# Performance work log

Hardware: AMD Instinct MI355X
Metric: run time of the kernel (lower is better)

## Reference

```python
import jax, jax.numpy as jnp
import numpy as np

N_FFT = 2048
HOP = 512
OUT_CH = N_FFT // 2 + 1  # 1025


def _dft_conv_weights():
    # periodic ('fftbins=True') Hann window, win_length == n_fft so no padding
    n = np.arange(N_FFT)
    window = 0.5 - 0.5 * np.cos(2.0 * np.pi * n / N_FFT)
    k = np.arange(OUT_CH)
    ang = 2.0 * np.pi * np.outer(k, n) / N_FFT  # (OUT_CH, N_FFT)
    w_real = (np.cos(ang) * window[None, :]).astype(np.float32)
    w_imag = (-np.sin(ang) * window[None, :]).astype(np.float32)
    return jnp.asarray(w_real), jnp.asarray(w_imag)


def setup_inputs() -> dict:
    key = jax.random.key(0)
    x = jax.random.normal(key, (32, 2, 160000), dtype=jnp.float32)
    W_real, W_imag = _dft_conv_weights()
    return {"x": x, "W_real": W_real, "W_imag": W_imag}


def reference(x, W_real, W_imag):
    # x: (B, C, L). center=True -> reflect pad by n_fft//2 on both sides.
    pad = N_FFT // 2
    x_pad = jnp.pad(x, ((0, 0), (0, 0), (pad, pad)), mode="reflect")
    L = x_pad.shape[-1]
    num_frames = (L - N_FFT) // HOP + 1  # 313
    # frame indices: (T, N_FFT)
    idx = jnp.arange(num_frames)[:, None] * HOP + jnp.arange(N_FFT)[None, :]
    frames = x_pad[..., idx]  # (B, C, T, N_FFT)
    # windowed DFT as matmul (equivalent to the Conv1d with stride=hop)
    real = jnp.einsum("bctn,kn->bctk", frames, W_real)
    imag = jnp.einsum("bctn,kn->bctk", frames, W_imag)
    return real, imag
```

## Files before the change

### kernel.cpp

```cpp
#include <hip/hip_runtime.h>

#define B_     32
#define C_     2
#define L_     160000
#define HOP    512
#define PAD    1024
#define LPAD   162048
#define T_     313
#define BC     64
#define M_     20032
#define KCH    1025
#define OUT_HALF 20532800UL
#define PL     81024
#define KD     1024
#define ND     1024
#define NKT    32
#define MTP    160
#define NWG    1280
#define LIMW   8336

typedef __attribute__((ext_vector_type(8))) short short8;
typedef __attribute__((ext_vector_type(4))) float f32x4;

static __device__ __forceinline__ short f2bf(float f) {
  union { float f; unsigned u; } v; v.f = f;
  unsigned u = v.u;
  unsigned r = (u + 0x7fffu + ((u >> 16) & 1u)) >> 16;
  return (short)r;
}

__global__ void prep_planes(const float* __restrict__ x,
                            short* __restrict__ pl0, short* __restrict__ pl1) {
  int v = blockIdx.x * 256 + threadIdx.x;
  int bc = v / 10128;
  int r  = v - bc * 10128;
  int p0 = r * 8;
  const float* src = x + (size_t)bc * L_;
  short8 e, o;
  if (r >= 64 && r <= 10000) {
    int j0 = 16 * r - 1024;
    #pragma unroll
    for (int qq = 0; qq < 4; ++qq) {
      float4 f = *(const float4*)(src + j0 + qq * 4);
      e[qq * 2 + 0] = f2bf(f.x); o[qq * 2 + 0] = f2bf(f.y);
      e[qq * 2 + 1] = f2bf(f.z); o[qq * 2 + 1] = f2bf(f.w);
    }
  } else {
    #pragma unroll
    for (int u = 0; u < 16; ++u) {
      int j = 16 * r + u - 1024;
      j = j < 0 ? -j : j;
      j = j >= L_ ? 2 * L_ - 2 - j : j;
      short b = f2bf(src[j]);
      if (u & 1) o[u >> 1] = b; else e[u >> 1] = b;
    }
  }
  *(short8*)&pl0[(size_t)bc * PL + p0] = e;
  *(short8*)&pl1[(size_t)bc * PL + p0] = o;
}

__global__ void prep_wb(short* __restrict__ wb0, short* __restrict__ wb1) {
  int id = blockIdx.x * 256 + threadIdx.x;
  int s   = id >> 17;
  int row = (id >> 7) & 1023;
  int n8  = (id & 127) * 8;
  int kp  = row >> 1, e = row & 1;
  short8 ov;
  #pragma unroll
  for (int u = 0; u < 8; ++u) {
    int n1 = n8 + u;
    float win = 0.5f - 0.5f * cosf((float)(2 * n1 + s) * 3.0679615757712823e-3f);
    float tw;
    if (e == 0)       tw = cosf((float)((n1 * kp) & 1023) * 6.1359231515425649e-3f);
    else if (kp == 0) tw = (n1 & 1) ? -1.0f : 1.0f;
    else              tw = -sinf((float)((n1 * kp) & 1023) * 6.1359231515425649e-3f);
    ov[u] = f2bf(win * tw);
  }
  short* wb = s ? wb1 : wb0;
  *(short8*)&wb[(size_t)row * KD + n8] = ov;
}

#define GLOAD16(g, l) __builtin_amdgcn_global_load_lds(                        \
    (const __attribute__((address_space(1))) void*)(g),                        \
    (__attribute__((address_space(3))) void*)(l), 16, 0, 0)

__global__ __launch_bounds__(512, 4) void stft_gemm(const short* __restrict__ pl0,
                                                    const short* __restrict__ pl1,
                                                    const short* __restrict__ wb0,
                                                    const short* __restrict__ wb1,
                                                    float* __restrict__ out) {
  __shared__ __align__(16) char lds[66688];
  const int tid  = threadIdx.x;
  const int lane = tid & 63;
  const int wid  = tid >> 6;

  const int id = blockIdx.x;
  const int mt = (id & 7) * 20 + (id >> 6);
  const int nt = (id >> 3) & 7;
  const int M0 = mt * 128, N0 = nt * 128;

  const int srow = tid >> 2;
  const int chunkSwz = ((tid & 3) ^ ((tid >> 3) & 3)) * 8;
  const short* aP[2];
  const short* bP[2];
  {
    int m = M0 + srow; if (m > M_ - 1) m = M_ - 1;
    int bc = m / T_;
    int t  = m - bc * T_;
    size_t base = (size_t)bc * PL + (size_t)t * 256 + chunkSwz;
    aP[0] = pl0 + base;
    aP[1] = pl1 + base;
    size_t bb = (size_t)(N0 + srow) * KD + chunkSwz;
    bP[0] = wb0 + bb;
    bP[1] = wb1 + bb;
  }
  const int dstOff = tid * 16;

  const int wr = wid >> 2, wc = wid & 3;
  const int fr = lane & 15;
  const int xorb = ((lane >> 4) * 16) ^ ((fr & 6) << 3);
  int afOff[2][4], bfOff[2][2];
  #pragma unroll
  for (int s = 0; s < 2; ++s) {
    #pragma unroll
    for (int i = 0; i < 4; ++i)
      afOff[s][i] = s * 8192 + (wr * 64 + i * 16 + fr) * 64 + xorb;
    #pragma unroll
    for (int j = 0; j < 2; ++j)
      bfOff[s][j] = 16384 + s * 8192 + (wc * 32 + j * 16 + fr) * 64 + xorb;
  }

  f32x4 acc[2][4][2];
  #pragma unroll
  for (int s = 0; s < 2; ++s)
    #pragma unroll
    for (int i = 0; i < 4; ++i)
      #pragma unroll
      for (int j = 0; j < 2; ++j) acc[s][i][j] = (f32x4){0.f, 0.f, 0.f, 0.f};

  GLOAD16(aP[0], lds + dstOff);
  GLOAD16(bP[0], lds + 16384 + dstOff);
  GLOAD16(aP[1], lds + 8192 + dstOff);
  GLOAD16(bP[1], lds + 24576 + dstOff);

  for (int kt = 0; kt < NKT; ++kt) {
    char* bufR = lds + (kt & 1) * 32768;
    char* bufW = lds + ((kt + 1) & 1) * 32768;
    const int kos = (kt + 1) * 32;
    const bool st = (kt < NKT - 1);

    asm volatile("s_waitcnt vmcnt(2)" ::: "memory");
    __builtin_amdgcn_s_barrier();
    if (st) {
      GLOAD16(aP[0] + kos, bufW + dstOff);
      GLOAD16(bP[0] + kos, bufW + 16384 + dstOff);
    }
    short8 af0[4], bf0[2];
    #pragma unroll
    for (int i = 0; i < 4; ++i) af0[i] = *(const short8*)(bufR + afOff[0][i]);
    #pragma unroll
    for (int j = 0; j < 2; ++j) bf0[j] = *(const short8*)(bufR + bfOff[0][j]);
    __builtin_amdgcn_s_barrier();
    __builtin_amdgcn_s_setprio(1);
    #pragma unroll
    for (int i = 0; i < 4; ++i)
      #pragma unroll
      for (int j = 0; j < 2; ++j)
        acc[0][i][j] = __builtin_amdgcn_mfma_f32_16x16x32_bf16(af0[i], bf0[j],
                                                               acc[0][i][j], 0, 0, 0);
    __builtin_amdgcn_s_setprio(0);

    if (st) asm volatile("s_waitcnt vmcnt(2)" ::: "memory");
    else    asm volatile("s_waitcnt vmcnt(0)" ::: "memory");
    __builtin_amdgcn_s_barrier();
    if (st) {
      GLOAD16(aP[1] + kos, bufW + 8192 + dstOff);
      GLOAD16(bP[1] + kos, bufW + 24576 + dstOff);
    }
    short8 af1[4], bf1[2];
    #pragma unroll
    for (int i = 0; i < 4; ++i) af1[i] = *(const short8*)(bufR + afOff[1][i]);
    #pragma unroll
    for (int j = 0; j < 2; ++j) bf1[j] = *(const short8*)(bufR + bfOff[1][j]);
    __builtin_amdgcn_s_barrier();
    __builtin_amdgcn_s_setprio(1);
    #pragma unroll
    for (int i = 0; i < 4; ++i)
      #pragma unroll
      for (int j = 0; j < 2; ++j)
        acc[1][i][j] = __builtin_amdgcn_mfma_f32_16x16x32_bf16(af1[i], bf1[j],
                                                               acc[1][i][j], 0, 0, 0);
    __builtin_amdgcn_s_setprio(0);
  }

  float* L = (float*)lds;
  float* outI = out + OUT_HALF;
  const float PIQ = 3.0679615757712823e-3f;
  const int rgrp = (lane >> 4) << 2;

  __syncthreads();

  #pragma unroll
  for (int pass = 0; pass < 2; ++pass) {
    #pragma unroll
    for (int j = 0; j < 2; ++j) {
      int c  = wc * 32 + j * 16 + fr;
      int q  = c >> 1;
      int qg = nt * 64 + q;
      float ang = (float)qg * PIQ;
      float tr = cosf(ang), sn = sinf(ang);
      bool odd  = c & 1;
      bool spec = (nt == 0) && (c == 1);
      float sgn = odd ? -sn : sn;
      int widx = (odd ? LIMW : 0) + (pass ? (63 - q) : q);
      #pragma unroll
      for (int i = 0; i < 4; ++i) {
        int row = wr * 64 + i * 16 + rgrp;
        #pragma unroll
        for (int r = 0; r < 4; ++r) {
          float v0 = acc[0][i][j][r];
          float v1 = acc[1][i][j][r];
          float p1 = __shfl_xor(v1, 1);
          float u  = tr * v1 + sgn * p1;
          float val;
          if (pass == 0) val = v0 + u;
          else           val = odd ? -(v0 - u) : (v0 - u);
          if (spec) val = 0.f;
          L[widx + (row + r) * 65] = val;
          if (spec && pass == 0) {
            int gm = M0 + row + r;
            if (gm < M_) {
              out [(size_t)gm * KCH + 512] = v0;
              outI[(size_t)gm * KCH + 512] = -v1;
            }
          }
        }
      }
    }
    __syncthreads();
    {
      int col0 = pass ? (1024 - nt * 64 - 63) : (nt * 64);
      #pragma unroll
      for (int i2 = 0; i2 < 16; ++i2) {
        int row = wid + i2 * 8;
        int gm  = M0 + row;
        if (gm < M_) {
          size_t rb = (size_t)gm * KCH + col0 + lane;
          out [rb] = L[row * 65 + lane];
          outI[rb] = L[LIMW + row * 65 + lane];
        }
      }
    }
    __syncthreads();
  }
}

extern "C" void kernel_launch(void* const* d_in, const int* in_sizes, int n_in,
                              void* d_out, int out_size, void* d_ws, size_t ws_size,
                              hipStream_t stream) {
  const float* x = (const float*)d_in[0];
  float* out = (float*)d_out;

  short* pl0 = (short*)d_ws;
  short* pl1 = pl0 + (size_t)BC * PL;
  short* wb0 = pl1 + (size_t)BC * PL;
  short* wb1 = wb0 + (size_t)ND * KD;

  prep_planes<<<2532, 256, 0, stream>>>(x, pl0, pl1);
  prep_wb<<<1024, 256, 0, stream>>>(wb0, wb1);

  stft_gemm<<<NWG, 512, 0, stream>>>(pl0, pl1, wb0, wb1, out);
}
```

Baseline: 139.1 us.

## Split even/odd sub-GEMMs across warp halves with 64x64 warp tiles

Each warp now computes one of the two sub-sums (even or odd sample plane) over a 64x64 output tile, instead of both sub-sums over a 64x32 tile. This raises MFMA count per LDS fragment load and lets all four global-to-LDS loads per k-step be issued together behind one wait and barrier pair instead of two. The epilogue becomes two phases: even-plane warps write their partial results to LDS, then after a barrier the odd-plane warps apply the twiddle and accumulate into LDS. The cost is an extra barrier and read-modify-write in the epilogue, and the k-loop prefetch now completes one full stage ahead with a vmcnt wait that changes the overlap pattern.

```diff
diff --git a/kernel.cpp b/kernel.cpp
--- a/kernel.cpp
+++ b/kernel.cpp
@@ -13,7 +13,6 @@
 #define OUT_HALF 20532800UL
 #define PL     81024
 #define KD     1024
-#define ND     1024
 #define NKT    32
 #define MTP    160
 #define NWG    1280
@@ -99,49 +98,44 @@
   const int nt = (id >> 3) & 7;
   const int M0 = mt * 128, N0 = nt * 128;
 
-  const int srow = tid >> 2;
-  const int chunkSwz = ((tid & 3) ^ ((tid >> 3) & 3)) * 8;
-  const short* aP[2];
-  const short* bP[2];
+  const int sw = wid & 1, wn = (wid >> 1) & 1, wm = wid >> 2;
+
+  const int srow  = tid >> 2;
+  const int chunk = ((tid & 3) ^ ((tid >> 3) & 3)) * 8;
+  const short *a0S, *a1S, *b0S, *b1S;
   {
     int m = M0 + srow; if (m > M_ - 1) m = M_ - 1;
     int bc = m / T_;
     int t  = m - bc * T_;
-    size_t base = (size_t)bc * PL + (size_t)t * 256 + chunkSwz;
-    aP[0] = pl0 + base;
-    aP[1] = pl1 + base;
-    size_t bb = (size_t)(N0 + srow) * KD + chunkSwz;
-    bP[0] = wb0 + bb;
-    bP[1] = wb1 + bb;
-  }
-  const int dstOff = tid * 16;
-
-  const int wr = wid >> 2, wc = wid & 3;
+    size_t base = (size_t)bc * PL + (size_t)t * 256 + chunk;
+    a0S = pl0 + base;
+    a1S = pl1 + base;
+    size_t bb = (size_t)(N0 + srow) * KD + chunk;
+    b0S = wb0 + bb;
+    b1S = wb1 + bb;
+  }
+  const int dst = tid * 16;
+
   const int fr = lane & 15;
   const int xorb = ((lane >> 4) * 16) ^ ((fr & 6) << 3);
-  int afOff[2][4], bfOff[2][2];
-  #pragma unroll
-  for (int s = 0; s < 2; ++s) {
-    #pragma unroll
-    for (int i = 0; i < 4; ++i)
-      afOff[s][i] = s * 8192 + (wr * 64 + i * 16 + fr) * 64 + xorb;
-    #pragma unroll
-    for (int j = 0; j < 2; ++j)
-      bfOff[s][j] = 16384 + s * 8192 + (wc * 32 + j * 16 + fr) * 64 + xorb;
-  }
-
-  f32x4 acc[2][4][2];
-  #pragma unroll
-  for (int s = 0; s < 2; ++s)
-    #pragma unroll
-    for (int i = 0; i < 4; ++i)
-      #pragma unroll
-      for (int j = 0; j < 2; ++j) acc[s][i][j] = (f32x4){0.f, 0.f, 0.f, 0.f};
-
-  GLOAD16(aP[0], lds + dstOff);
-  GLOAD16(bP[0], lds + 16384 + dstOff);
-  GLOAD16(aP[1], lds + 8192 + dstOff);
-  GLOAD16(bP[1], lds + 24576 + dstOff);
+  int aOff[4], bOff[4];
+  #pragma unroll
+  for (int i = 0; i < 4; ++i)
+    aOff[i] = sw * 8192 + (wm * 64 + i * 16 + fr) * 64 + xorb;
+  #pragma unroll
+  for (int j = 0; j < 4; ++j)
+    bOff[j] = 16384 + sw * 8192 + (wn * 64 + j * 16 + fr) * 64 + xorb;
+
+  f32x4 acc[4][4];
+  #pragma unroll
+  for (int i = 0; i < 4; ++i)
+    #pragma unroll
+    for (int j = 0; j < 4; ++j) acc[i][j] = (f32x4){0.f, 0.f, 0.f, 0.f};
+
+  GLOAD16(a0S, lds + dst);
+  GLOAD16(a1S, lds + 8192 + dst);
+  GLOAD16(b0S, lds + 16384 + dst);
+  GLOAD16(b1S, lds + 24576 + dst);
 
   for (int kt = 0; kt < NKT; ++kt) {
     char* bufR = lds + (kt & 1) * 32768;
@@ -149,48 +143,31 @@
     const int kos = (kt + 1) * 32;
     const bool st = (kt < NKT - 1);
 
-    asm volatile("s_waitcnt vmcnt(2)" ::: "memory");
+    if (st) {
+      GLOAD16(a0S + kos, bufW + dst);
+      GLOAD16(a1S + kos, bufW + 8192 + dst);
+      GLOAD16(b0S + kos, bufW + 16384 + dst);
+      GLOAD16(b1S + kos, bufW + 24576 + dst);
+      asm volatile("s_waitcnt vmcnt(4)" ::: "memory");
+    } else {
+      asm volatile("s_waitcnt vmcnt(0)" ::: "memory");
+    }
     __builtin_amdgcn_s_barrier();
-    if (st) {
-      GLOAD16(aP[0] + kos, bufW + dstOff);
-      GLOAD16(bP[0] + kos, bufW + 16384 + dstOff);
-    }
-    short8 af0[4], bf0[2];
-    #pragma unroll
-    for (int i = 0; i < 4; ++i) af0[i] = *(const short8*)(bufR + afOff[0][i]);
-    #pragma unroll
-    for (int j = 0; j < 2; ++j) bf0[j] = *(const short8*)(bufR + bfOff[0][j]);
+
+    short8 af[4], bf[4];
+    #pragma unroll
+    for (int i = 0; i < 4; ++i) af[i] = *(const short8*)(bufR + aOff[i]);
+    #pragma unroll
+    for (int j = 0; j < 4; ++j) bf[j] = *(const short8*)(bufR + bOff[j]);
+    __builtin_amdgcn_s_setprio(1);
+    #pragma unroll
+    for (int i = 0; i < 4; ++i)
+      #pragma unroll
+      for (int j = 0; j < 4; ++j)
+        acc[i][j] = __builtin_amdgcn_mfma_f32_16x16x32_bf16(af[i], bf[j],
+                                                            acc[i][j], 0, 0, 0);
+    __builtin_amdgcn_s_setprio(0);
     __builtin_amdgcn_s_barrier();
-    __builtin_amdgcn_s_setprio(1);
-    #pragma unroll
-    for (int i = 0; i < 4; ++i)
-      #pragma unroll
-      for (int j = 0; j < 2; ++j)
-        acc[0][i][j] = __builtin_amdgcn_mfma_f32_16x16x32_bf16(af0[i], bf0[j],
-                                                               acc[0][i][j], 0, 0, 0);
-    __builtin_amdgcn_s_setprio(0);
-
-    if (st) asm volatile("s_waitcnt vmcnt(2)" ::: "memory");
-    else    asm volatile("s_waitcnt vmcnt(0)" ::: "memory");
-    __builtin_amdgcn_s_barrier();
-    if (st) {
-      GLOAD16(aP[1] + kos, bufW + 8192 + dstOff);
-      GLOAD16(bP[1] + kos, bufW + 24576 + dstOff);
-    }
-    short8 af1[4], bf1[2];
-    #pragma unroll
-    for (int i = 0; i < 4; ++i) af1[i] = *(const short8*)(bufR + afOff[1][i]);
-    #pragma unroll
-    for (int j = 0; j < 2; ++j) bf1[j] = *(const short8*)(bufR + bfOff[1][j]);
-    __builtin_amdgcn_s_barrier();
-    __builtin_amdgcn_s_setprio(1);
-    #pragma unroll
-    for (int i = 0; i < 4; ++i)
-      #pragma unroll
-      for (int j = 0; j < 2; ++j)
-        acc[1][i][j] = __builtin_amdgcn_mfma_f32_16x16x32_bf16(af1[i], bf1[j],
-                                                               acc[1][i][j], 0, 0, 0);
-    __builtin_amdgcn_s_setprio(0);
   }
 
   float* L = (float*)lds;
@@ -202,36 +179,58 @@
 
   #pragma unroll
   for (int pass = 0; pass < 2; ++pass) {
-    #pragma unroll
-    for (int j = 0; j < 2; ++j) {
-      int c  = wc * 32 + j * 16 + fr;
-      int q  = c >> 1;
-      int qg = nt * 64 + q;
-      float ang = (float)qg * PIQ;
-      float tr = cosf(ang), sn = sinf(ang);
-      bool odd  = c & 1;
-      bool spec = (nt == 0) && (c == 1);
-      float sgn = odd ? -sn : sn;
-      int widx = (odd ? LIMW : 0) + (pass ? (63 - q) : q);
-      #pragma unroll
-      for (int i = 0; i < 4; ++i) {
-        int row = wr * 64 + i * 16 + rgrp;
+    if (sw == 0) {
+      #pragma unroll
+      for (int j = 0; j < 4; ++j) {
+        int c  = wn * 64 + j * 16 + fr;
+        int q  = c >> 1;
+        bool odd  = c & 1;
+        bool spec = (nt == 0) && (c == 1);
+        int widx = (odd ? LIMW : 0) + (pass ? (63 - q) : q);
         #pragma unroll
-        for (int r = 0; r < 4; ++r) {
-          float v0 = acc[0][i][j][r];
-          float v1 = acc[1][i][j][r];
-          float p1 = __shfl_xor(v1, 1);
-          float u  = tr * v1 + sgn * p1;
-          float val;
-          if (pass == 0) val = v0 + u;
-          else           val = odd ? -(v0 - u) : (v0 - u);
-          if (spec) val = 0.f;
-          L[widx + (row + r) * 65] = val;
-          if (spec && pass == 0) {
-            int gm = M0 + row + r;
-            if (gm < M_) {
-              out [(size_t)gm * KCH + 512] = v0;
-              outI[(size_t)gm * KCH + 512] = -v1;
+        for (int i = 0; i < 4; ++i) {
+          int row = wm * 64 + i * 16 + rgrp;
+          #pragma unroll
+          for (int r = 0; r < 4; ++r) {
+            float v0 = acc[i][j][r];
+            float base = pass == 0 ? v0 : (odd ? -v0 : v0);
+            if (spec) base = 0.f;
+            L[widx + (row + r) * 65] = base;
+            if (spec && pass == 0) {
+              int gm = M0 + row + r;
+              if (gm < M_) out[(size_t)gm * KCH + 512] = v0;
+            }
+          }
+        }
+      }
+    }
+    __syncthreads();
+    if (sw == 1) {
+      #pragma unroll
+      for (int j = 0; j < 4; ++j) {
+        int c  = wn * 64 + j * 16 + fr;
+        int q  = c >> 1;
+        float ang = (float)(nt * 64 + q) * PIQ;
+        float tr = cosf(ang), sn = sinf(ang);
+        bool odd  = c & 1;
+        bool spec = (nt == 0) && (c == 1);
+        float sgn = odd ? -sn : sn;
+        int widx = (odd ? LIMW : 0) + (pass ? (63 - q) : q);
+        #pragma unroll
+        for (int i = 0; i < 4; ++i) {
+          int row = wm * 64 + i * 16 + rgrp;
+          #pragma unroll
+          for (int r = 0; r < 4; ++r) {
+            float v1 = acc[i][j][r];
+            float p1 = __shfl_xor(v1, 1);
+            float u  = tr * v1 + sgn * p1;
+            if (!spec) {
+              float addv = (pass == 0) ? u : (odd ? u : -u);
+              int li = widx + (row + r) * 65;
+              L[li] += addv;
+            } else if (pass == 0) {
+              int gm = M0 + row + r;
+              if (gm < M_) outI[(size_t)gm * KCH + 512] = -v1;
             }
           }
         }
@@ -264,7 +263,7 @@
   short* pl0 = (short*)d_ws;
   short* pl1 = pl0 + (size_t)BC * PL;
   short* wb0 = pl1 + (size_t)BC * PL;
-  short* wb1 = wb0 + (size_t)ND * KD;
+  short* wb1 = wb0 + (size_t)1024 * KD;
 
   prep_planes<<<2532, 256, 0, stream>>>(x, pl0, pl1);
   prep_wb<<<1024, 256, 0, stream>>>(wb0, wb1);
```

Result: slower. 147.8 us (+6.3%).

## Double M tile to 256 rows with triple-buffered LDS software pipeline

Applied to the files above, without the earlier changes.

Each workgroup now computes a 256x128 output tile instead of 128x128, which halves the grid and doubles per-wave accumulators (8x2 per plane). The K loop switches from a two-buffer scheme with split barriers to a three-slot LDS ring that prefetches two stages ahead and interleaves fragment loads with MFMA issue. This aims to raise B-tile reuse and hide global-load latency, at the cost of more registers, more LDS (~144KB) and lower occupancy (launch bounds 2), plus a smaller grid that may underfill the CUs.

```diff
diff --git a/kernel.cpp b/kernel.cpp
--- a/kernel.cpp
+++ b/kernel.cpp
@@ -3,9 +3,6 @@
 #define B_     32
 #define C_     2
 #define L_     160000
-#define HOP    512
-#define PAD    1024
-#define LPAD   162048
 #define T_     313
 #define BC     64
 #define M_     20032
@@ -13,11 +10,10 @@
 #define OUT_HALF 20532800UL
 #define PL     81024
 #define KD     1024
-#define ND     1024
 #define NKT    32
-#define MTP    160
-#define NWG    1280
-#define LIMW   8336
+#define NWG    640
+#define SLOT   49152
+#define IMBASE 16640
 
 typedef __attribute__((ext_vector_type(8))) short short8;
 typedef __attribute__((ext_vector_type(4))) float f32x4;
@@ -84,119 +80,125 @@
     (const __attribute__((address_space(1))) void*)(g),                        \
     (__attribute__((address_space(3))) void*)(l), 16, 0, 0)
 
-__global__ __launch_bounds__(512, 4) void stft_gemm(const short* __restrict__ pl0,
+__global__ __launch_bounds__(512, 2) void stft_gemm(const short* __restrict__ pl0,
                                                     const short* __restrict__ pl1,
                                                     const short* __restrict__ wb0,
                                                     const short* __restrict__ wb1,
                                                     float* __restrict__ out) {
-  __shared__ __align__(16) char lds[66688];
+  __shared__ __align__(16) char lds[3 * SLOT];
   const int tid  = threadIdx.x;
   const int lane = tid & 63;
   const int wid  = tid >> 6;
 
   const int id = blockIdx.x;
-  const int mt = (id & 7) * 20 + (id >> 6);
+  const int mt = (id & 7) * 10 + (id >> 6);
   const int nt = (id >> 3) & 7;
-  const int M0 = mt * 128, N0 = nt * 128;
-
-  const int srow = tid >> 2;
-  const int chunkSwz = ((tid & 3) ^ ((tid >> 3) & 3)) * 8;
-  const short* aP[2];
-  const short* bP[2];
-  {
-    int m = M0 + srow; if (m > M_ - 1) m = M_ - 1;
+  const int M0 = mt * 256;
+  const int wm = wid >> 2, wn = wid & 3;
+
+  const int srow  = tid >> 2;
+  const int chunk = ((tid & 3) ^ ((tid >> 3) & 3)) * 8;
+  const short* aS[2][2];
+  const short* bS[2];
+  #pragma unroll
+  for (int h = 0; h < 2; ++h) {
+    int m = M0 + h * 128 + srow; if (m > M_ - 1) m = M_ - 1;
     int bc = m / T_;
     int t  = m - bc * T_;
-    size_t base = (size_t)bc * PL + (size_t)t * 256 + chunkSwz;
-    aP[0] = pl0 + base;
-    aP[1] = pl1 + base;
-    size_t bb = (size_t)(N0 + srow) * KD + chunkSwz;
-    bP[0] = wb0 + bb;
-    bP[1] = wb1 + bb;
-  }
-  const int dstOff = tid * 16;
-
-  const int wr = wid >> 2, wc = wid & 3;
-  const int fr = lane & 15;
-  const int xorb = ((lane >> 4) * 16) ^ ((fr & 6) << 3);
-  int afOff[2][4], bfOff[2][2];
-  #pragma unroll
-  for (int s = 0; s < 2; ++s) {
-    #pragma unroll
-    for (int i = 0; i < 4; ++i)
-      afOff[s][i] = s * 8192 + (wr * 64 + i * 16 + fr) * 64 + xorb;
+    size_t base = (size_t)bc * PL + (size_t)t * 256 + chunk;
+    aS[0][h] = pl0 + base;
+    aS[1][h] = pl1 + base;
+  }
+  {
+    int n = nt * 128 + srow;
+    size_t bb = (size_t)n * KD + chunk;
+    bS[0] = wb0 + bb;
+    bS[1] = wb1 + bb;
+  }
+  const int dst = tid * 16;
+
+  const int fr = lane & 15, kh = lane >> 4;
+  const int xorb = (kh * 16) ^ ((fr & 6) << 3);
+  int aOff[2][8], bOff[2][2];
+  #pragma unroll
+  for (int p = 0; p < 2; ++p) {
+    #pragma unroll
+    for (int i = 0; i < 8; ++i)
+      aOff[p][i] = p * 16384 + (wm * 128 + i * 16 + fr) * 64 + xorb;
     #pragma unroll
     for (int j = 0; j < 2; ++j)
-      bfOff[s][j] = 16384 + s * 8192 + (wc * 32 + j * 16 + fr) * 64 + xorb;
-  }
-
-  f32x4 acc[2][4][2];
-  #pragma unroll
-  for (int s = 0; s < 2; ++s)
-    #pragma unroll
-    for (int i = 0; i < 4; ++i)
-      #pragma unroll
-      for (int j = 0; j < 2; ++j) acc[s][i][j] = (f32x4){0.f, 0.f, 0.f, 0.f};
-
-  GLOAD16(aP[0], lds + dstOff);
-  GLOAD16(bP[0], lds + 16384 + dstOff);
-  GLOAD16(aP[1], lds + 8192 + dstOff);
-  GLOAD16(bP[1], lds + 24576 + dstOff);
+      bOff[p][j] = 32768 + p * 8192 + (wn * 32 + j * 16 + fr) * 64 + xorb;
+  }
+
+  f32x4 acc0[8][2], acc1[8][2];
+  #pragma unroll
+  for (int i = 0; i < 8; ++i)
+    #pragma unroll
+    for (int j = 0; j < 2; ++j) {
+      acc0[i][j] = (f32x4){0.f, 0.f, 0.f, 0.f};
+      acc1[i][j] = (f32x4){0.f, 0.f, 0.f, 0.f};
+    }
+
+  #define STAGE(S, KO) do { char* s_ = (S); const int ko_ = (KO);              \
+      GLOAD16(aS[0][0] + ko_, s_ + dst);                                       \
+      GLOAD16(aS[0][1] + ko_, s_ + 8192  + dst);                               \
+      GLOAD16(aS[1][0] + ko_, s_ + 16384 + dst);                               \
+      GLOAD16(aS[1][1] + ko_, s_ + 24576 + dst);                               \
+      GLOAD16(bS[0]    + ko_, s_ + 32768 + dst);                               \
+      GLOAD16(bS[1]    + ko_, s_ + 40960 + dst); } while (0)
+
+  STAGE(lds, 0);
+  STAGE(lds + SLOT, 32);
+  asm volatile("s_waitcnt vmcnt(6)" ::: "memory");
+  __builtin_amdgcn_s_barrier();
+
+  short8 af0[8], af1[8], bf0[2], bf1[2];
+  #pragma unroll
+  for (int i = 0; i < 8; ++i) af0[i] = *(const short8*)(lds + aOff[0][i]);
+  #pragma unroll
+  for (int j = 0; j < 2; ++j) bf0[j] = *(const short8*)(lds + bOff[0][j]);
 
   for (int kt = 0; kt < NKT; ++kt) {
-    char* bufR = lds + (kt & 1) * 32768;
-    char* bufW = lds + ((kt + 1) & 1) * 32768;
-    const int kos = (kt + 1) * 32;
-    const bool st = (kt < NKT - 1);
-
-    asm volatile("s_waitcnt vmcnt(2)" ::: "memory");
+    char* sR = lds + (kt % 3) * SLOT;
+
+    if (kt + 2 < NKT) STAGE(lds + ((kt + 2) % 3) * SLOT, (kt + 2) * 32);
+    #pragma unroll
+    for (int i = 0; i < 8; ++i) af1[i] = *(const short8*)(sR + aOff[1][i]);
+    #pragma unroll
+    for (int j = 0; j < 2; ++j) bf1[j] = *(const short8*)(sR + bOff[1][j]);
+    __builtin_amdgcn_s_setprio(1);
+    #pragma unroll
+    for (int i = 0; i < 8; ++i)
+      #pragma unroll
+      for (int j = 0; j < 2; ++j)
+        acc0[i][j] = __builtin_amdgcn_mfma_f32_16x16x32_bf16(af0[i], bf0[j],
+                                                             acc0[i][j], 0, 0, 0);
+    __builtin_amdgcn_s_setprio(0);
+
+    if (kt + 2 < NKT)      asm volatile("s_waitcnt vmcnt(6)" ::: "memory");
+    else if (kt + 1 < NKT) asm volatile("s_waitcnt vmcnt(0)" ::: "memory");
+    asm volatile("s_waitcnt lgkmcnt(0)" ::: "memory");
     __builtin_amdgcn_s_barrier();
-    if (st) {
-      GLOAD16(aP[0] + kos, bufW + dstOff);
-      GLOAD16(bP[0] + kos, bufW + 16384 + dstOff);
-    }
-    short8 af0[4], bf0[2];
-    #pragma unroll
-    for (int i = 0; i < 4; ++i) af0[i] = *(const short8*)(bufR + afOff[0][i]);
-    #pragma unroll
-    for (int j = 0; j < 2; ++j) bf0[j] = *(const short8*)(bufR + bfOff[0][j]);
-    __builtin_amdgcn_s_barrier();
+    if (kt + 1 < NKT) {
+      char* sN = lds + ((kt + 1) % 3) * SLOT;
+      #pragma unroll
+      for (int i = 0; i < 8; ++i) af0[i] = *(const short8*)(sN + aOff[0][i]);
+      #pragma unroll
+      for (int j = 0; j < 2; ++j) bf0[j] = *(const short8*)(sN + bOff[0][j]);
+    }
     __builtin_amdgcn_s_setprio(1);
     #pragma unroll
-    for (int i = 0; i < 4; ++i)
+    for (int i = 0; i < 8; ++i)
       #pragma unroll
       for (int j = 0; j < 2; ++j)
-        acc[0][i][j] = __builtin_amdgcn_mfma_f32_16x16x32_bf16(af0[i], bf0[j],
-                                                               acc[0][i][j], 0, 0, 0);
+        acc1[i][j] = __builtin_amdgcn_mfma_f32_16x16x32_bf16(af1[i], bf1[j],
+                                                             acc1[i][j], 0, 0, 0);
     __builtin_amdgcn_s_setprio(0);
-
-    if (st) asm volatile("s_waitcnt vmcnt(2)" ::: "memory");
-    else    asm volatile("s_waitcnt vmcnt(0)" ::: "memory");
-    __builtin_amdgcn_s_barrier();
-    if (st) {
-      GLOAD16(aP[1] + kos, bufW + 8192 + dstOff);
-      GLOAD16(bP[1] + kos, bufW + 24576 + dstOff);
-    }
-    short8 af1[4], bf1[2];
-    #pragma unroll
-    for (int i = 0; i < 4; ++i) af1[i] = *(const short8*)(bufR + afOff[1][i]);
-    #pragma unroll
-    for (int j = 0; j < 2; ++j) bf1[j] = *(const short8*)(bufR + bfOff[1][j]);
-    __builtin_amdgcn_s_barrier();
-    __builtin_amdgcn_s_setprio(1);
-    #pragma unroll
-    for (int i = 0; i < 4; ++i)
-      #pragma unroll
-      for (int j = 0; j < 2; ++j)
-        acc[1][i][j] = __builtin_amdgcn_mfma_f32_16x16x32_bf16(af1[i], bf1[j],
-                                                               acc[1][i][j], 0, 0, 0);
-    __builtin_amdgcn_s_setprio(0);
-  }
-
-  float* L = (float*)lds;
+  }
+
+  float* Lf = (float*)lds;
   float* outI = out + OUT_HALF;
   const float PIQ = 3.0679615757712823e-3f;
-  const int rgrp = (lane >> 4) << 2;
 
   __syncthreads();
 
@@ -204,31 +206,28 @@
   for (int pass = 0; pass < 2; ++pass) {
     #pragma unroll
     for (int j = 0; j < 2; ++j) {
-      int c  = wc * 32 + j * 16 + fr;
+      int c  = wn * 32 + j * 16 + fr;
       int q  = c >> 1;
-      int qg = nt * 64 + q;
-      float ang = (float)qg * PIQ;
+      float ang = (float)(nt * 64 + q) * PIQ;
       float tr = cosf(ang), sn = sinf(ang);
       bool odd  = c & 1;
       bool spec = (nt == 0) && (c == 1);
       float sgn = odd ? -sn : sn;
-      int widx = (odd ? LIMW : 0) + (pass ? (63 - q) : q);
-      #pragma unroll
-      for (int i = 0; i < 4; ++i) {
-        int row = wr * 64 + i * 16 + rgrp;
+      int fidx = (odd ? IMBASE : 0) + (pass ? (63 - q) : q);
+      #pragma unroll
+      for (int i = 0; i < 8; ++i) {
+        int grow = wm * 128 + i * 16 + kh * 4;
         #pragma unroll
         for (int r = 0; r < 4; ++r) {
-          float v0 = acc[0][i][j][r];
-          float v1 = acc[1][i][j][r];
+          float v0 = acc0[i][j][r];
+          float v1 = acc1[i][j][r];
           float p1 = __shfl_xor(v1, 1);
           float u  = tr * v1 + sgn * p1;
-          float val;
-          if (pass == 0) val = v0 + u;
-          else           val = odd ? -(v0 - u) : (v0 - u);
+          float val = (pass == 0) ? (v0 + u) : (odd ? -(v0 - u) : (v0 - u));
           if (spec) val = 0.f;
-          L[widx + (row + r) * 65] = val;
+          Lf[fidx + (grow + r) * 65] = val;
           if (spec && pass == 0) {
-            int gm = M0 + row + r;
+            int gm = M0 + grow + r;
             if (gm < M_) {
               out [(size_t)gm * KCH + 512] = v0;
               outI[(size_t)gm * KCH + 512] = -v1;
@@ -241,13 +240,13 @@
     {
       int col0 = pass ? (1024 - nt * 64 - 63) : (nt * 64);
       #pragma unroll
-      for (int i2 = 0; i2 < 16; ++i2) {
+      for (int i2 = 0; i2 < 32; ++i2) {
         int row = wid + i2 * 8;
         int gm  = M0 + row;
         if (gm < M_) {
           size_t rb = (size_t)gm * KCH + col0 + lane;
-          out [rb] = L[row * 65 + lane];
-          outI[rb] = L[LIMW + row * 65 + lane];
+          out [rb] = Lf[row * 65 + lane];
+          outI[rb] = Lf[IMBASE + row * 65 + lane];
         }
       }
     }
@@ -264,7 +263,7 @@
   short* pl0 = (short*)d_ws;
   short* pl1 = pl0 + (size_t)BC * PL;
   short* wb0 = pl1 + (size_t)BC * PL;
-  short* wb1 = wb0 + (size_t)ND * KD;
+  short* wb1 = wb0 + (size_t)1024 * KD;
 
   prep_planes<<<2532, 256, 0, stream>>>(x, pl0, pl1);
   prep_wb<<<1024, 256, 0, stream>>>(wb0, wb1);
```

New measurement: 151.1 us. 1.09x slower.
